# Optimization experiments

Measured on AMD Instinct MI355X. Metric: run time of the kernel, lower is better.

The kernel has to match this reference:

```python
import jax, jax.numpy as jnp
import numpy as np

B, T, D_IN, H, NUM_CLASSES = 512, 1024, 4, 64, 1098


def setup_inputs() -> dict:
    key = jax.random.key(0)
    ks = jax.random.split(key, 20)
    s = 1.0 / np.sqrt(H)  # PyTorch LSTM init range

    def w(k, shape):
        return jax.random.uniform(k, shape, jnp.float32, -s, s)

    inp = {}
    inp['x'] = jax.random.normal(ks[0], (B, T, D_IN), jnp.float32)
    lens = jax.random.randint(ks[1], (B,), 1, T + 1)
    inp['lengths'] = jnp.sort(lens)[::-1]  # descending, like pack_sequence
    i = 2
    for layer, d in ((0, D_IN), (1, 2 * H)):
        for dirn in ('f', 'b'):
            inp[f'W_ih_l{layer}{dirn}'] = w(ks[i], (4 * H, d)); i += 1
            inp[f'W_hh_l{layer}{dirn}'] = w(ks[i], (4 * H, H)); i += 1
            inp[f'b_ih_l{layer}{dirn}'] = w(ks[i], (4 * H,)); i += 1
            inp[f'b_hh_l{layer}{dirn}'] = w(ks[i], (4 * H,)); i += 1
    inp['W_out'] = w(ks[i], (NUM_CLASSES, 2 * H)); i += 1
    inp['b_out'] = w(ks[i], (NUM_CLASSES,))
    return inp


def _lstm_layer(x, W_ih, W_hh, b_ih, b_hh):
    # x: [B, T, D] -> outputs [B, T, H]; PyTorch gate order i, f, g, o
    Bb = x.shape[0]
    Hh = W_hh.shape[1]
    xW = jnp.einsum('btd,gd->btg', x, W_ih) + b_ih + b_hh  # [B, T, 4H]

    def step(carry, xt):
        h, c = carry
        g = xt + h @ W_hh.T
        i, f, gg, o = jnp.split(g, 4, axis=-1)
        c = jax.nn.sigmoid(f) * c + jax.nn.sigmoid(i) * jnp.tanh(gg)
        h = jax.nn.sigmoid(o) * jnp.tanh(c)
        return (h, c), h

    init = (jnp.zeros((Bb, Hh), x.dtype), jnp.zeros((Bb, Hh), x.dtype))
    _, hs = jax.lax.scan(step, init, jnp.swapaxes(xW, 0, 1))
    return jnp.swapaxes(hs, 0, 1)


def _reverse_padded(x, lengths):
    # per-sequence time reversal within the valid length (packed-seq semantics)
    Tt = x.shape[1]
    t = jnp.arange(Tt)
    idx = jnp.where(t[None, :] < lengths[:, None], lengths[:, None] - 1 - t[None, :], t[None, :])
    return jnp.take_along_axis(x, idx[:, :, None], axis=1)


def _bidir_layer(x, lengths, pf, pb):
    hf = _lstm_layer(x, *pf)
    hb = _reverse_padded(_lstm_layer(_reverse_padded(x, lengths), *pb), lengths)
    return jnp.concatenate([hf, hb], axis=-1)


def reference(x, lengths,
              W_ih_l0f, W_hh_l0f, b_ih_l0f, b_hh_l0f,
              W_ih_l0b, W_hh_l0b, b_ih_l0b, b_hh_l0b,
              W_ih_l1f, W_hh_l1f, b_ih_l1f, b_hh_l1f,
              W_ih_l1b, W_hh_l1b, b_ih_l1b, b_hh_l1b,
              W_out, b_out):
    h = _bidir_layer(x, lengths,
                     (W_ih_l0f, W_hh_l0f, b_ih_l0f, b_hh_l0f),
                     (W_ih_l0b, W_hh_l0b, b_ih_l0b, b_hh_l0b))
    h = _bidir_layer(h, lengths,
                     (W_ih_l1f, W_hh_l1f, b_ih_l1f, b_hh_l1f),
                     (W_ih_l1b, W_hh_l1b, b_ih_l1b, b_hh_l1b))
    # gather last valid timestep per sequence: [B, 2H]
    lasts = jnp.take_along_axis(h, (lengths - 1)[:, None, None], axis=1)[:, 0]
    return lasts @ W_out.T + b_out
```

## Files before the change

kernel.cpp:

```cpp
#include <hip/hip_runtime.h>
#include <stdint.h>

#define BATCH 512
#define TMAX 1024
#define DIN 4
#define H 64
#define NC 1098
#define RCH 32

typedef __attribute__((ext_vector_type(2))) float v2;

__device__ __forceinline__ v2 mkv2(float a, float b) { v2 r; r.x = a; r.y = b; return r; }

__device__ __forceinline__ float sigmoidf_(float x) {
    return 1.0f / (1.0f + __expf(-x));
}
__device__ __forceinline__ float tanhf_(float x) {
    return 1.0f - 2.0f / (__expf(2.0f * x) + 1.0f);
}
__device__ __forceinline__ uint32_t f2bf(float f) {
    uint32_t u = __float_as_uint(f);
    return (u + 0x7FFFu + ((u >> 16) & 1u)) >> 16;
}
__device__ __forceinline__ float bf2f(uint32_t h) {
    return __uint_as_float(h << 16);
}

__global__ __launch_bounds__(128) void lstm_layer0_p2(
    const float* __restrict__ x, const int* __restrict__ lengths,
    const float* __restrict__ Wih_f, const float* __restrict__ Whh_f,
    const float* __restrict__ bih_f, const float* __restrict__ bhh_f,
    const float* __restrict__ Wih_b, const float* __restrict__ Whh_b,
    const float* __restrict__ bih_b, const float* __restrict__ bhh_b,
    uint16_t* __restrict__ h0b )
{
    const int unit = blockIdx.x;
    const int b = unit >> 1, dir = unit & 1;
    const int t = threadIdx.x;
    const int j = t & 63, w = t >> 6;
    const int L = lengths[b];

    const float* Wih = dir ? Wih_b : Wih_f;
    const float* Whh = dir ? Whh_b : Whh_f;
    const float* bih = dir ? bih_b : bih_f;
    const float* bhh = dir ? bhh_b : bhh_f;

    const int rA = (2*w) * H + j;
    const int rB = (2*w + 1) * H + j;

    v2 wA[32], wB[32];
    {
        const float4* pa = (const float4*)(Whh + (size_t)rA * H);
        const float4* pb = (const float4*)(Whh + (size_t)rB * H);
        #pragma unroll
        for (int k = 0; k < 16; k++) {
            float4 va = pa[k], vb = pb[k];
            wA[2*k] = mkv2(va.x, va.y); wA[2*k+1] = mkv2(va.z, va.w);
            wB[2*k] = mkv2(vb.x, vb.y); wB[2*k+1] = mkv2(vb.z, vb.w);
        }
    }
    const float4 wxA = ((const float4*)Wih)[rA];
    const float4 wxB = ((const float4*)Wih)[rB];
    const float bA = bih[rA] + bhh[rA];
    const float bB = bih[rB] + bhh[rB];

    __shared__ __align__(16) float4 xbuf4[TMAX];
    __shared__ __align__(16) float hist[32 * H];
    __shared__ __align__(16) float hrep[2][H];
    __shared__ __align__(16) v2 ex2[2][2][H];

    {
        const float4* x4 = (const float4*)x + (size_t)b * TMAX;
        for (int i = t; i < L; i += 128) xbuf4[i] = x4[i];
    }
    hrep[w][j] = 0.0f;
    float c = 0.0f;
    __syncthreads();

    for (int s = 0; s < L; s++) {
        const int tt = dir ? (L - 1 - s) : s;
        const float4 xt = xbuf4[tt];

        v2 aA0 = mkv2(bA, 0.0f), aA1 = mkv2(0.0f, 0.0f);
        v2 aB0 = mkv2(bB, 0.0f), aB1 = mkv2(0.0f, 0.0f);
        {
            v2 xlo = mkv2(xt.x, xt.y), xhi = mkv2(xt.z, xt.w);
            aA0 += mkv2(wxA.x, wxA.y) * xlo; aA1 += mkv2(wxA.z, wxA.w) * xhi;
            aB0 += mkv2(wxB.x, wxB.y) * xlo; aB1 += mkv2(wxB.z, wxB.w) * xhi;
        }
        const float4* h4 = (const float4*)hrep[w];
        #pragma unroll
        for (int k = 0; k < 16; k++) {
            float4 hv = h4[k];
            v2 hlo = mkv2(hv.x, hv.y), hhi = mkv2(hv.z, hv.w);
            aA0 += wA[2*k] * hlo; aA1 += wA[2*k+1] * hhi;
            aB0 += wB[2*k] * hlo; aB1 += wB[2*k+1] * hhi;
        }
        const float aAs = (aA0.x + aA0.y) + (aA1.x + aA1.y);
        const float aBs = (aB0.x + aB0.y) + (aB1.x + aB1.y);
        const float actA = (w == 1) ? tanhf_(aAs) : sigmoidf_(aAs);
        const float actB = sigmoidf_(aBs);
        const int p = s & 1;
        ex2[p][w][j] = mkv2(actA, actB);
        __syncthreads();
        const v2 other = ex2[p][1 - w][j];
        const float gi = w ? other.x : actA;
        const float gf = w ? other.y : actB;
        const float gg = w ? actA : other.x;
        const float go = w ? actB : other.y;
        c = fmaf(gf, c, gi * gg);
        const float h = go * tanhf_(c);
        hrep[w][j] = h;
        if (w == 0) {
            hist[(s & 31) * H + j] = h;
            if ((s & 31) == 31 || s == L - 1) {
                const int s0c = s & ~31, nrows = s - s0c + 1;
                const int jc = j & 31, jr = j >> 5;
                for (int base = 0; base + jr < nrows; base += 2) {
                    const int rr = base + jr;
                    const int t2 = dir ? (L - 1 - (s0c + rr)) : (s0c + rr);
                    const float2 hv = *(const float2*)(hist + rr * H + jc * 2);
                    const uint32_t pk = f2bf(hv.x) | (f2bf(hv.y) << 16);
                    *(uint32_t*)(h0b + ((size_t)b * TMAX + t2) * (2*H) + dir * H + jc * 2) = pk;
                }
            }
        }
    }
}

__global__ __launch_bounds__(512) void lstm_rec_pipe(
    const uint16_t* __restrict__ h0b, const int* __restrict__ lengths,
    const float* __restrict__ Wih, const float* __restrict__ Whh,
    const float* __restrict__ bih, const float* __restrict__ bhh,
    const float* __restrict__ Wih_b,
    const float* __restrict__ bih_b, const float* __restrict__ bhh_b,
    const float* __restrict__ Wout, const float* __restrict__ bout,
    float* __restrict__ out)
{
    const int b = blockIdx.x;
    const int t = threadIdx.x;
    const int j = t & 63, w = t >> 6;
    const int L = lengths[b];
    const bool isProd = (w < 4);

    __shared__ __align__(16) float xch[RCH * 128];
    __shared__ __align__(16) float part[2][4][256];
    __shared__ __align__(16) float hrep[4][H];
    __shared__ __align__(16) float ex[2][4][H];
    __shared__ __align__(16) float ybuf[2*H];

    v2 wreg[64];
    float bias = 0.0f;
    if (isProd) {
        #pragma unroll
        for (int q = 0; q < 4; q++) {
            const float4* pw = (const float4*)(Wih + (size_t)(4*j + q) * 128 + 32 * w);
            #pragma unroll
            for (int k = 0; k < 8; k++) {
                float4 v = pw[k];
                wreg[q*16 + 2*k]     = mkv2(v.x, v.y);
                wreg[q*16 + 2*k + 1] = mkv2(v.z, v.w);
            }
        }
    } else {
        const int g = (w - 4) * H + j;
        const float4* pw = (const float4*)(Whh + (size_t)g * H);
        #pragma unroll
        for (int k = 0; k < 16; k++) {
            float4 v = pw[k];
            wreg[2*k]     = mkv2(v.x, v.y);
            wreg[2*k + 1] = mkv2(v.z, v.w);
        }
        bias = bih[g] + bhh[g];
        hrep[w - 4][j] = 0.0f;
    }
    float c = 0.0f, h = 0.0f;

    auto produce = [&](int r, int p) {
        const float4* xr = (const float4*)(xch + r * 128 + 32 * w);
        v2 a0 = mkv2(0,0), a1 = mkv2(0,0), a2 = mkv2(0,0), a3 = mkv2(0,0);
        #pragma unroll
        for (int k = 0; k < 8; k++) {
            float4 xv = xr[k];
            v2 xlo = mkv2(xv.x, xv.y), xhi = mkv2(xv.z, xv.w);
            a0 += wreg[ 0 + 2*k] * xlo; a0 += wreg[ 0 + 2*k + 1] * xhi;
            a1 += wreg[16 + 2*k] * xlo; a1 += wreg[16 + 2*k + 1] * xhi;
            a2 += wreg[32 + 2*k] * xlo; a2 += wreg[32 + 2*k + 1] * xhi;
            a3 += wreg[48 + 2*k] * xlo; a3 += wreg[48 + 2*k + 1] * xhi;
        }
        *(float4*)&part[p][w][4*j] =
            make_float4(a0.x + a0.y, a1.x + a1.y, a2.x + a2.y, a3.x + a3.y);
    };

    for (int s = 0; s < L; s++) {
        const int rr = s & (RCH - 1);
        if (rr == 0) {
            __syncthreads();
            const uint32_t* src = (const uint32_t*)(h0b + ((size_t)b * TMAX + s) * (2*H));
            for (int i = t; i < RCH * 64; i += 512) {
                uint32_t u = src[i];
                *(float2*)(xch + 2*i) = make_float2(bf2f(u & 0xFFFFu), bf2f(u >> 16));
            }
            __syncthreads();
            if (isProd) produce(0, s & 1);
            __syncthreads();
        }
        if (isProd) {
            if (s + 1 < L && rr + 1 < RCH)
                produce(rr + 1, (s + 1) & 1);
        } else {
            const int g = (w - 4) * H + j;
            const float pa = part[s & 1][0][g] + part[s & 1][1][g]
                           + part[s & 1][2][g] + part[s & 1][3][g];
            v2 a0 = mkv2(pa + bias, 0.0f), a1 = mkv2(0.0f, 0.0f);
            const float4* h4 = (const float4*)hrep[w - 4];
            #pragma unroll
            for (int k = 0; k < 16; k++) {
                float4 hv = h4[k];
                a0 += wreg[2*k]     * mkv2(hv.x, hv.y);
                a1 += wreg[2*k + 1] * mkv2(hv.z, hv.w);
            }
            const float a = (a0.x + a0.y) + (a1.x + a1.y);
            ex[s & 1][w - 4][j] = (w == 6) ? tanhf_(a) : sigmoidf_(a);
        }
        __syncthreads();
        if (!isProd) {
            const int p = s & 1;
            const float gi = ex[p][0][j], gf = ex[p][1][j];
            const float gg = ex[p][2][j], go = ex[p][3][j];
            c = fmaf(gf, c, gi * gg);
            h = go * tanhf_(c);
            hrep[w - 4][j] = h;
        }
    }

    if (w == 4) ybuf[j] = h;
    __syncthreads();
    const float* xrow = xch + ((L - 1) & (RCH - 1)) * 128;
    float* gb = &part[0][0][0];
    if (t < 256) {
        const float4* wb = (const float4*)(Wih_b + (size_t)t * 128);
        const float4* xv = (const float4*)xrow;
        v2 a0 = mkv2(bih_b[t] + bhh_b[t], 0.0f), a1 = mkv2(0.0f, 0.0f);
        #pragma unroll
        for (int k = 0; k < 32; k++) {
            float4 wv = wb[k], xk = xv[k];
            a0 += mkv2(wv.x, wv.y) * mkv2(xk.x, xk.y);
            a1 += mkv2(wv.z, wv.w) * mkv2(xk.z, xk.w);
        }
        const float a = (a0.x + a0.y) + (a1.x + a1.y);
        gb[t] = (t >= 128 && t < 192) ? tanhf_(a) : sigmoidf_(a);
    }
    __syncthreads();
    if (t < 64) {
        const float gi = gb[t], gg = gb[128 + t], go = gb[192 + t];
        ybuf[H + t] = go * tanhf_(gi * gg);
    }
    __syncthreads();

    const float4* yv = (const float4*)ybuf;
    for (int o = t; o < NC; o += 512) {
        const float4* wr = (const float4*)(Wout + (size_t)o * (2*H));
        v2 a0 = mkv2(bout[o], 0.0f), a1 = mkv2(0.0f, 0.0f);
        #pragma unroll
        for (int k = 0; k < 32; k++) {
            float4 wv = wr[k], yy = yv[k];
            a0 += mkv2(wv.x, wv.y) * mkv2(yy.x, yy.y);
            a1 += mkv2(wv.z, wv.w) * mkv2(yy.z, yy.w);
        }
        out[(size_t)b * NC + o] = (a0.x + a0.y) + (a1.x + a1.y);
    }
}

extern "C" void kernel_launch(void* const* d_in, const int* in_sizes, int n_in,
                              void* d_out, int out_size, void* d_ws, size_t ws_size,
                              hipStream_t stream) {
    const float* x        = (const float*)d_in[0];
    const int*   lengths  = (const int*)  d_in[1];
    const float* Wih_l0f  = (const float*)d_in[2];
    const float* Whh_l0f  = (const float*)d_in[3];
    const float* bih_l0f  = (const float*)d_in[4];
    const float* bhh_l0f  = (const float*)d_in[5];
    const float* Wih_l0b  = (const float*)d_in[6];
    const float* Whh_l0b  = (const float*)d_in[7];
    const float* bih_l0b  = (const float*)d_in[8];
    const float* bhh_l0b  = (const float*)d_in[9];
    const float* Wih_l1f  = (const float*)d_in[10];
    const float* Whh_l1f  = (const float*)d_in[11];
    const float* bih_l1f  = (const float*)d_in[12];
    const float* bhh_l1f  = (const float*)d_in[13];
    const float* Wih_l1b  = (const float*)d_in[14];
    const float* bih_l1b  = (const float*)d_in[16];
    const float* bhh_l1b  = (const float*)d_in[17];
    const float* Wout     = (const float*)d_in[18];
    const float* bout     = (const float*)d_in[19];
    float* out = (float*)d_out;

    uint16_t* h0b = (uint16_t*)d_ws;

    lstm_layer0_p2<<<dim3(2 * BATCH), 128, 0, stream>>>(
        x, lengths,
        Wih_l0f, Whh_l0f, bih_l0f, bhh_l0f,
        Wih_l0b, Whh_l0b, bih_l0b, bhh_l0b, h0b);

    lstm_rec_pipe<<<dim3(BATCH), 512, 0, stream>>>(
        h0b, lengths,
        Wih_l1f, Whh_l1f, bih_l1f, bhh_l1f,
        Wih_l1b, bih_l1b, bhh_l1b, Wout, bout, out);
}
```

Before: 1.428 ms.

## Compute all four gates per thread in layer-0 LSTM, removing per-step block barrier

The layer-0 kernel now launches one block per batch element, with one wavefront per direction. Each thread holds all four gate rows of W_hh in registers (256 floats) and computes every gate itself. This removes the cross-wavefront gate exchange and the __syncthreads on every timestep. Because the hidden state is then written and read within a single wavefront, there is no barrier between the write of h and the next step's read. The batched bf16 output staging through shared memory is also replaced by a direct strided 2-byte store each step. The trade-offs are much higher register pressure (launch bounds 128,1), less parallelism per step, and uncoalesced per-step global writes.

```diff
diff --git a/kernel.cpp b/kernel.cpp
--- a/kernel.cpp
+++ b/kernel.cpp
@@ -2,31 +2,24 @@
 #include <stdint.h>
 
 #define BATCH 512
-#define TMAX 1024
-#define DIN 4
-#define H 64
-#define NC 1098
-#define RCH 32
+#define TMAX  1024
+#define DIN   4
+#define H     64
+#define NC    1098
+#define RCH   32
 
 typedef __attribute__((ext_vector_type(2))) float v2;
 
 __device__ __forceinline__ v2 mkv2(float a, float b) { v2 r; r.x = a; r.y = b; return r; }
-
-__device__ __forceinline__ float sigmoidf_(float x) {
-    return 1.0f / (1.0f + __expf(-x));
-}
-__device__ __forceinline__ float tanhf_(float x) {
-    return 1.0f - 2.0f / (__expf(2.0f * x) + 1.0f);
-}
+__device__ __forceinline__ float sigmoidf_(float x) { return 1.0f / (1.0f + __expf(-x)); }
+__device__ __forceinline__ float tanhf_(float x) { return 1.0f - 2.0f / (__expf(2.0f * x) + 1.0f); }
 __device__ __forceinline__ uint32_t f2bf(float f) {
     uint32_t u = __float_as_uint(f);
     return (u + 0x7FFFu + ((u >> 16) & 1u)) >> 16;
 }
-__device__ __forceinline__ float bf2f(uint32_t h) {
-    return __uint_as_float(h << 16);
-}
-
-__global__ __launch_bounds__(128) void lstm_layer0_p2(
+__device__ __forceinline__ float bf2f(uint32_t h) { return __uint_as_float(h << 16); }
+
+__global__ __launch_bounds__(128, 1) void lstm_l0(
     const float* __restrict__ x, const int* __restrict__ lengths,
     const float* __restrict__ Wih_f, const float* __restrict__ Whh_f,
     const float* __restrict__ bih_f, const float* __restrict__ bhh_f,
@@ -34,10 +27,9 @@
     const float* __restrict__ bih_b, const float* __restrict__ bhh_b,
     uint16_t* __restrict__ h0b )
 {
-    const int unit = blockIdx.x;
-    const int b = unit >> 1, dir = unit & 1;
+    const int b = blockIdx.x;
     const int t = threadIdx.x;
-    const int j = t & 63, w = t >> 6;
+    const int j = t & 63, dir = t >> 6;
     const int L = lengths[b];
 
     const float* Wih = dir ? Wih_b : Wih_f;
@@ -45,86 +37,68 @@
     const float* bih = dir ? bih_b : bih_f;
     const float* bhh = dir ? bhh_b : bhh_f;
 
-    const int rA = (2*w) * H + j;
-    const int rB = (2*w + 1) * H + j;
-
-    v2 wA[32], wB[32];
-    {
-        const float4* pa = (const float4*)(Whh + (size_t)rA * H);
-        const float4* pb = (const float4*)(Whh + (size_t)rB * H);
+    v2 w[4][32];
+    #pragma unroll
+    for (int g = 0; g < 4; g++) {
+        const float4* pw = (const float4*)(Whh + (size_t)(64*g + j) * H);
         #pragma unroll
         for (int k = 0; k < 16; k++) {
-            float4 va = pa[k], vb = pb[k];
-            wA[2*k] = mkv2(va.x, va.y); wA[2*k+1] = mkv2(va.z, va.w);
-            wB[2*k] = mkv2(vb.x, vb.y); wB[2*k+1] = mkv2(vb.z, vb.w);
-        }
-    }
-    const float4 wxA = ((const float4*)Wih)[rA];
-    const float4 wxB = ((const float4*)Wih)[rB];
-    const float bA = bih[rA] + bhh[rA];
-    const float bB = bih[rB] + bhh[rB];
-
-    __shared__ __align__(16) float4 xbuf4[TMAX];
-    __shared__ __align__(16) float hist[32 * H];
-    __shared__ __align__(16) float hrep[2][H];
-    __shared__ __align__(16) v2 ex2[2][2][H];
-
+            float4 a = pw[k];
+            w[g][2*k]   = mkv2(a.x, a.y);
+            w[g][2*k+1] = mkv2(a.z, a.w);
+        }
+    }
+    float4 wx[4]; float bb[4];
+    #pragma unroll
+    for (int g = 0; g < 4; g++) {
+        wx[g] = ((const float4*)Wih)[64*g + j];
+        bb[g] = bih[64*g + j] + bhh[64*g + j];
+    }
+
+    __shared__ __align__(16) float4 xbuf[TMAX];
+    __shared__ __align__(16) float  hbc[2][H];
     {
         const float4* x4 = (const float4*)x + (size_t)b * TMAX;
-        for (int i = t; i < L; i += 128) xbuf4[i] = x4[i];
-    }
-    hrep[w][j] = 0.0f;
+        for (int i = t; i < L; i += 128) xbuf[i] = x4[i];
+    }
+    hbc[dir][j] = 0.0f;
     float c = 0.0f;
     __syncthreads();
+
+    uint16_t* outp = h0b + (size_t)b * TMAX * (2*H) + dir * H + j;
 
     for (int s = 0; s < L; s++) {
         const int tt = dir ? (L - 1 - s) : s;
-        const float4 xt = xbuf4[tt];
-
-        v2 aA0 = mkv2(bA, 0.0f), aA1 = mkv2(0.0f, 0.0f);
-        v2 aB0 = mkv2(bB, 0.0f), aB1 = mkv2(0.0f, 0.0f);
-        {
-            v2 xlo = mkv2(xt.x, xt.y), xhi = mkv2(xt.z, xt.w);
-            aA0 += mkv2(wxA.x, wxA.y) * xlo; aA1 += mkv2(wxA.z, wxA.w) * xhi;
-            aB0 += mkv2(wxB.x, wxB.y) * xlo; aB1 += mkv2(wxB.z, wxB.w) * xhi;
-        }
-        const float4* h4 = (const float4*)hrep[w];
+        const float4 xt = xbuf[tt];
+        float p[4];
+        #pragma unroll
+        for (int g = 0; g < 4; g++)
+            p[g] = fmaf(wx[g].w, xt.w, fmaf(wx[g].z, xt.z,
+                   fmaf(wx[g].y, xt.y, fmaf(wx[g].x, xt.x, bb[g]))));
+        v2 a0[4], a1[4];
+        #pragma unroll
+        for (int g = 0; g < 4; g++) { a0[g] = mkv2(0.f,0.f); a1[g] = mkv2(0.f,0.f); }
+        const float4* h4 = (const float4*)hbc[dir];
         #pragma unroll
         for (int k = 0; k < 16; k++) {
             float4 hv = h4[k];
-            v2 hlo = mkv2(hv.x, hv.y), hhi = mkv2(hv.z, hv.w);
-            aA0 += wA[2*k] * hlo; aA1 += wA[2*k+1] * hhi;
-            aB0 += wB[2*k] * hlo; aB1 += wB[2*k+1] * hhi;
-        }
-        const float aAs = (aA0.x + aA0.y) + (aA1.x + aA1.y);
-        const float aBs = (aB0.x + aB0.y) + (aB1.x + aB1.y);
-        const float actA = (w == 1) ? tanhf_(aAs) : sigmoidf_(aAs);
-        const float actB = sigmoidf_(aBs);
-        const int p = s & 1;
-        ex2[p][w][j] = mkv2(actA, actB);
-        __syncthreads();
-        const v2 other = ex2[p][1 - w][j];
-        const float gi = w ? other.x : actA;
-        const float gf = w ? other.y : actB;
-        const float gg = w ? actA : other.x;
-        const float go = w ? actB : other.y;
+            v2 lo = mkv2(hv.x, hv.y), hi = mkv2(hv.z, hv.w);
+            #pragma unroll
+            for (int g = 0; g < 4; g++) {
+                a0[g] += w[g][2*k]   * lo;
+                a1[g] += w[g][2*k+1] * hi;
+            }
+        }
+        #pragma unroll
+        for (int g = 0; g < 4; g++) { v2 sv = a0[g] + a1[g]; p[g] += sv.x + sv.y; }
+        const float gi = sigmoidf_(p[0]);
+        const float gf = sigmoidf_(p[1]);
+        const float gg = tanhf_(p[2]);
+        const float go = sigmoidf_(p[3]);
         c = fmaf(gf, c, gi * gg);
         const float h = go * tanhf_(c);
-        hrep[w][j] = h;
-        if (w == 0) {
-            hist[(s & 31) * H + j] = h;
-            if ((s & 31) == 31 || s == L - 1) {
-                const int s0c = s & ~31, nrows = s - s0c + 1;
-                const int jc = j & 31, jr = j >> 5;
-                for (int base = 0; base + jr < nrows; base += 2) {
-                    const int rr = base + jr;
-                    const int t2 = dir ? (L - 1 - (s0c + rr)) : (s0c + rr);
-                    const float2 hv = *(const float2*)(hist + rr * H + jc * 2);
-                    const uint32_t pk = f2bf(hv.x) | (f2bf(hv.y) << 16);
-                    *(uint32_t*)(h0b + ((size_t)b * TMAX + t2) * (2*H) + dir * H + jc * 2) = pk;
-                }
-            }
-        }
+        hbc[dir][j] = h;
+        outp[(size_t)tt * (2*H)] = (uint16_t)f2bf(h);
     }
 }
 
@@ -298,7 +272,7 @@
 
     uint16_t* h0b = (uint16_t*)d_ws;
 
-    lstm_layer0_p2<<<dim3(2 * BATCH), 128, 0, stream>>>(
+    lstm_l0<<<dim3(BATCH), 128, 0, stream>>>(
         x, lengths,
         Wih_l0f, Whh_l0f, bih_l0f, bhh_l0f,
         Wih_l0b, Whh_l0b, bih_l0b, bhh_l0b, h0b);
```

Measured after the change: 1.797 ms. 1.26x slower.
